# Kernel optimization log

Measured on AMD Instinct MI355X. Metric: run time of the kernel, lower is better.

## Reference

```python
import jax, jax.numpy as jnp
import numpy as np

B, N, D, S, ITERS = 64, 4096, 256, 8, 3
EPS_ATTN = 1e-8
EPS_LN = 1e-5


def layernorm(x, g, b):
    mu = jnp.mean(x, axis=-1, keepdims=True)
    var = jnp.mean(jnp.square(x - mu), axis=-1, keepdims=True)
    return (x - mu) * jax.lax.rsqrt(var + EPS_LN) * g + b


def setup_inputs() -> dict:
    key = jax.random.key(0)
    ks = jax.random.split(key, 12)
    inputs = jax.random.normal(ks[0], (B, N, D), jnp.float32)
    mask = jax.random.randint(ks[1], (B, N), 0, 2) == 1  # bool, True = masked out
    # xavier-normal init for slots parameter [S, D]
    slots_init = jax.random.normal(ks[2], (S, D), jnp.float32) * np.sqrt(2.0 / (S + D))
    w_std = np.sqrt(1.0 / D)
    Wq = jax.random.normal(ks[3], (D, D), jnp.float32) * w_std
    bq = jnp.zeros((D,), jnp.float32)
    Wk = jax.random.normal(ks[4], (D, D), jnp.float32) * w_std
    bk = jnp.zeros((D,), jnp.float32)
    Wv = jax.random.normal(ks[5], (D, D), jnp.float32) * w_std
    bv = jnp.zeros((D,), jnp.float32)
    W1 = jax.random.normal(ks[6], (D, D), jnp.float32) * w_std
    b1 = jnp.zeros((D,), jnp.float32)
    W2 = jax.random.normal(ks[7], (D, D), jnp.float32) * w_std
    b2 = jnp.zeros((D,), jnp.float32)
    g_in, b_in = jnp.ones((D,)), jnp.zeros((D,))
    g_s, b_s = jnp.ones((D,)), jnp.zeros((D,))
    g_m, b_m = jnp.ones((D,)), jnp.zeros((D,))
    g_o, b_o = jnp.ones((D,)), jnp.zeros((D,))
    return {
        "inputs": inputs, "mask": mask, "slots_init": slots_init,
        "g_in": g_in, "b_in": b_in, "g_s": g_s, "b_s": b_s,
        "g_m": g_m, "b_m": b_m, "g_o": g_o, "b_o": b_o,
        "Wq": Wq, "bq": bq, "Wk": Wk, "bk": bk, "Wv": Wv, "bv": bv,
        "W1": W1, "b1": b1, "W2": W2, "b2": b2,
    }


def reference(inputs, mask, slots_init, g_in, b_in, g_s, b_s, g_m, b_m, g_o, b_o,
              Wq, bq, Wk, bk, Wv, bv, W1, b1, W2, b2):
    x = layernorm(inputs, g_in, b_in)            # [B,N,D]
    k = x @ Wk + bk                               # [B,N,D]
    v = x @ Wv + bv                               # [B,N,D]
    slots = jnp.broadcast_to(slots_init, (B, S, D))
    scale = D ** -0.5
    neg_max = -jnp.finfo(inputs.dtype).max
    for _ in range(ITERS):
        slots_prev = slots
        s = layernorm(slots, g_s, b_s)
        q = s @ Wq + bq                           # [B,S,D]
        dots = jnp.einsum('bid,bjd->bij', q, k) * scale   # [B,S,N]
        dots = jnp.where(mask[:, None, :], neg_max, dots)
        attn = jax.nn.softmax(dots, axis=1)       # softmax over slots (unusual axis)
        attn = attn / (jnp.sum(attn, axis=-1, keepdims=True) + EPS_ATTN)
        updates = jnp.einsum('bjd,bij->bid', v, attn)     # [B,S,D]
        slots = slots_prev + updates
        h = layernorm(slots, g_m, b_m)
        h = jax.nn.relu(h @ W1 + b1) @ W2 + b2    # 2-layer MLP
        slots = slots + h
    return layernorm(slots, g_o, b_o)
```

## Files before the change

kernel.cpp:

```cpp
#include <hip/hip_runtime.h>
#include <stdint.h>

#define BB 64
#define NN 4096
#define DD 256
#define SS 8
#define NITER 3
#define NCHUNK 8
#define EPS_LN 1e-5f
#define EPS_ATTN 1e-8f

typedef __attribute__((ext_vector_type(4))) float fvec4;
typedef __attribute__((ext_vector_type(8))) __bf16 bf16x8;
typedef __attribute__((ext_vector_type(8))) unsigned short usvec8;
typedef __attribute__((ext_vector_type(4))) unsigned short usvec4;

__device__ __forceinline__ float bf2f(unsigned short u) {
  return __uint_as_float(((unsigned)u) << 16);
}
__device__ __forceinline__ unsigned short f2bf(float f) {
  unsigned u = __float_as_uint(f);
  u += 0x7FFFu + ((u >> 16) & 1u);
  return (unsigned short)(u >> 16);
}
__device__ __forceinline__ void async_copy16(void* ldsp, const void* gp) {
  __builtin_amdgcn_global_load_lds(
      (const __attribute__((address_space(1))) unsigned int*)gp,
      (__attribute__((address_space(3))) unsigned int*)ldsp, 16, 0, 0);
}

__global__ void k_sinit(const float* __restrict__ slots_init, float* __restrict__ slots) {
  int b = blockIdx.x, t = threadIdx.x;
  const fvec4* src = (const fvec4*)slots_init;
  fvec4* dst = (fvec4*)(slots + (size_t)b * SS * DD);
  for (int j = t; j < SS * DD / 4; j += 256) dst[j] = src[j];
}

__global__ void k_wprepT(const float* __restrict__ Wk, float* __restrict__ WkT) {
  __shared__ float tile[16][17];
  int bx = blockIdx.x, by = blockIdx.y, t = threadIdx.x;
  int r = t >> 4, c = t & 15;
  tile[r][c] = Wk[(size_t)(by * 16 + r) * DD + bx * 16 + c];
  __syncthreads();
  WkT[(size_t)(bx * 16 + r) * DD + by * 16 + c] = tile[c][r];
}

__launch_bounds__(256)
__global__ void k_wcomb(const float* __restrict__ Wq, const float* __restrict__ WkT,
                        const float* __restrict__ bq, const float* __restrict__ bk,
                        float* __restrict__ Wqk, float* __restrict__ bqk,
                        float* __restrict__ wqbk, float* __restrict__ bqbk) {
  __shared__ float wqrow[DD];
  __shared__ float red[4];
  const float sc = 0.0625f;
  int j = blockIdx.x, t = threadIdx.x;
  wqrow[t] = Wq[(size_t)j * DD + t];
  __syncthreads();
  float a = 0.f;
#pragma unroll 4
  for (int dk = 0; dk < DD; dk++) a += wqrow[dk] * WkT[(size_t)dk * DD + t];
  Wqk[(size_t)j * DD + t] = a * sc;
  float c = wqrow[t] * bk[t];
#pragma unroll
  for (int m = 32; m >= 1; m >>= 1) c += __shfl_xor(c, m);
  if ((t & 63) == 0) red[t >> 6] = c;
  __syncthreads();
  if (t == 0) wqbk[j] = sc * (red[0] + red[1] + red[2] + red[3]);
  if (j == 0) {
    float bb = 0.f;
#pragma unroll 4
    for (int dk = 0; dk < DD; dk++) bb += bq[dk] * WkT[(size_t)dk * DD + t];
    bqk[t] = bb * sc;
    __syncthreads();
    float c2 = bq[t] * bk[t];
#pragma unroll
    for (int m = 32; m >= 1; m >>= 1) c2 += __shfl_xor(c2, m);
    if ((t & 63) == 0) red[t >> 6] = c2;
    __syncthreads();
    if (t == 0) bqbk[0] = sc * (red[0] + red[1] + red[2] + red[3]);
  }
}

__launch_bounds__(256)
__global__ void k_lnx(const float* __restrict__ in, const float* __restrict__ g,
                      const float* __restrict__ bt, unsigned short* __restrict__ xbf) {
  int t = threadIdx.x;
  long row = (long)blockIdx.x * 32 + (t >> 3);
  int u = t & 7;
  const float* rp = in + row * DD;
  fvec4 v[8];
  float s = 0.f, s2 = 0.f;
#pragma unroll
  for (int j = 0; j < 8; j++) {
    v[j] = *(const fvec4*)(rp + j * 32 + u * 4);
    s += v[j].x + v[j].y + v[j].z + v[j].w;
    s2 += v[j].x * v[j].x + v[j].y * v[j].y + v[j].z * v[j].z + v[j].w * v[j].w;
  }
  s += __shfl_xor(s, 1); s2 += __shfl_xor(s2, 1);
  s += __shfl_xor(s, 2); s2 += __shfl_xor(s2, 2);
  s += __shfl_xor(s, 4); s2 += __shfl_xor(s2, 4);
  float mu = s / DD;
  float rs = rsqrtf(s2 / DD - mu * mu + EPS_LN);
#pragma unroll
  for (int j = 0; j < 8; j++) {
    fvec4 gg = *(const fvec4*)(g + j * 32 + u * 4);
    fvec4 bb = *(const fvec4*)(bt + j * 32 + u * 4);
    usvec4 o;
    o[0] = f2bf((v[j].x - mu) * rs * gg.x + bb.x);
    o[1] = f2bf((v[j].y - mu) * rs * gg.y + bb.y);
    o[2] = f2bf((v[j].z - mu) * rs * gg.z + bb.z);
    o[3] = f2bf((v[j].w - mu) * rs * gg.w + bb.w);
    *(usvec4*)&xbf[row * DD + j * 32 + u * 4] = o;
  }
}

__launch_bounds__(256, 2)
__global__ void k_slotq2(const float* __restrict__ slots, const float* __restrict__ g_s,
                         const float* __restrict__ b_s, const float* __restrict__ Wqk,
                         const float* __restrict__ bqk, const float* __restrict__ wqbk,
                         const float* __restrict__ bqbk, float* __restrict__ qk,
                         float* __restrict__ qb, float* __restrict__ colsum) {
  __shared__ float sl[SS][DD];
  __shared__ float part[8][SS][32];
  __shared__ float qbp[4][SS];
  int b = blockIdx.x, cg = blockIdx.y, t = threadIdx.x;
  if (cg == 0 && t < SS) colsum[b * SS + t] = 0.f;
  int row = t >> 5, seg = t & 31;
  {
    const float* sp = slots + (size_t)(b * SS + row) * DD + seg * 8;
    float v[8];
    float s = 0.f, s2 = 0.f;
#pragma unroll
    for (int e = 0; e < 8; e++) { v[e] = sp[e]; s += v[e]; s2 += v[e] * v[e]; }
#pragma unroll
    for (int m = 16; m >= 1; m >>= 1) { s += __shfl_xor(s, m); s2 += __shfl_xor(s2, m); }
    float mu = s / DD;
    float rs = rsqrtf(s2 / DD - mu * mu + EPS_LN);
#pragma unroll
    for (int e = 0; e < 8; e++) {
      int d = seg * 8 + e;
      sl[row][d] = (v[e] - mu) * rs * g_s[d] + b_s[d];
    }
  }
  __syncthreads();
  if (cg == 0) {
    float wb = wqbk[t];
    float c8[SS];
#pragma unroll
    for (int i = 0; i < SS; i++) c8[i] = sl[i][t] * wb;
#pragma unroll
    for (int m = 32; m >= 1; m >>= 1)
#pragma unroll
      for (int i = 0; i < SS; i++) c8[i] += __shfl_xor(c8[i], m);
    if ((t & 63) == 0) {
#pragma unroll
      for (int i = 0; i < SS; i++) qbp[t >> 6][i] = c8[i];
    }
  }
  int kq = t >> 5, c = t & 31;
  int colg = cg * 32 + c;
  float a[SS] = {};
#pragma unroll 8
  for (int kk = 0; kk < 32; kk++) {
    int k = kq * 32 + kk;
    float wv = Wqk[(size_t)k * DD + colg];
#pragma unroll
    for (int i = 0; i < SS; i++) a[i] += sl[i][k] * wv;
  }
#pragma unroll
  for (int i = 0; i < SS; i++) part[kq][i][c] = a[i];
  __syncthreads();
  {
    int i = t >> 5, c2 = t & 31;
    float s = 0.f;
#pragma unroll
    for (int kq2 = 0; kq2 < 8; kq2++) s += part[kq2][i][c2];
    int cg2 = cg * 32 + c2;
    qk[(size_t)(b * SS + i) * DD + cg2] = s + bqk[cg2];
  }
  if (cg == 0 && t < SS)
    qb[b * SS + t] = qbp[0][t] + qbp[1][t] + qbp[2][t] + qbp[3][t] + bqbk[0];
}

__launch_bounds__(256, 2)
__global__ void k_attn2(const unsigned short* __restrict__ xbf,
                        const float* __restrict__ qkb, const float* __restrict__ qb,
                        const int* __restrict__ mask,
                        float* __restrict__ colsum, float* __restrict__ upart) {
  __shared__ __attribute__((aligned(16))) unsigned short kt[2][64 * 256];
  __shared__ float aL[2][64 * 9];
  int b = blockIdx.y, chunk = blockIdx.x, t = threadIdx.x;
  int w = t >> 6, lane = t & 63;
  int n_base = chunk * 512;
  int cl15 = lane & 15, hg = lane >> 4;

  bf16x8 qf[8];
  {
    int qrow = cl15 < 8 ? cl15 : 0;
    const float* qp = qkb + (size_t)(b * SS + qrow) * DD;
#pragma unroll
    for (int kst = 0; kst < 8; kst++) {
      int d0 = kst * 32 + hg * 8;
      usvec8 uq;
      if (cl15 < 8) {
        fvec4 q0 = *(const fvec4*)(qp + d0);
        fvec4 q1 = *(const fvec4*)(qp + d0 + 4);
        uq[0] = f2bf(q0.x); uq[1] = f2bf(q0.y); uq[2] = f2bf(q0.z); uq[3] = f2bf(q0.w);
        uq[4] = f2bf(q1.x); uq[5] = f2bf(q1.y); uq[6] = f2bf(q1.z); uq[7] = f2bf(q1.w);
      } else {
        uq = (usvec8)0;
      }
      qf[kst] = __builtin_bit_cast(bf16x8, uq);
    }
  }
  float qadd[4];
#pragma unroll
  for (int e = 0; e < 4; e++) qadd[e] = qb[b * SS + (hg & 1) * 4 + e];

  float acc[SS][8] = {};
  float csum[4] = {};
  int ns = t >> 5;

  auto stage = [&](int c, int bb) {
    int r0 = n_base + c * 64;
#pragma unroll
    for (int j = 0; j < 8; j++) {
      int gidx = w * 512 + j * 64 + lane;
      int row = gidx >> 5, c16 = gidx & 31;
      async_copy16(&kt[bb][gidx * 8],
                   xbf + ((size_t)(b * NN + r0 + row)) * DD + ((c16 ^ (row & 7)) * 8));
    }
  };

  stage(0, 0);
  for (int c = 0; c < 8; c++) {
    int bb = c & 1, pb = c & 1;
    int r0 = n_base + c * 64;
    if (c < 7) {
      stage(c + 1, bb ^ 1);
      asm volatile("s_waitcnt vmcnt(8)" ::: "memory");
    } else {
      asm volatile("s_waitcnt vmcnt(0)" ::: "memory");
    }
    __builtin_amdgcn_sched_barrier(0);
    fvec4 S = {0.f, 0.f, 0.f, 0.f};
    int row_l = w * 16 + cl15;
#pragma unroll
    for (int kst = 0; kst < 8; kst++) {
      int c16 = (kst * 4 + hg) ^ (row_l & 7);
      bf16x8 bfk = *(const bf16x8*)&kt[bb][row_l * 256 + c16 * 8];
      S = __builtin_amdgcn_mfma_f32_16x16x32_bf16(qf[kst], bfk, S, 0, 0, 0);
    }
    S[0] += qadd[0]; S[1] += qadd[1]; S[2] += qadd[2]; S[3] += qadd[3];
    {
      float m4 = fmaxf(fmaxf(S[0], S[1]), fmaxf(S[2], S[3]));
      float mo = __shfl_xor(m4, 16);
      float mx = fmaxf(m4, mo);
      float e0 = __expf(S[0] - mx), e1 = __expf(S[1] - mx);
      float e2 = __expf(S[2] - mx), e3 = __expf(S[3] - mx);
      float s4 = e0 + e1 + e2 + e3;
      float so = __shfl_xor(s4, 16);
      float inv = 1.f / (s4 + so);
      int mk = mask[(size_t)b * NN + r0 + row_l];
      float a0 = mk ? 0.125f : e0 * inv;
      float a1 = mk ? 0.125f : e1 * inv;
      float a2 = mk ? 0.125f : e2 * inv;
      float a3 = mk ? 0.125f : e3 * inv;
      if (lane < 32) {
        csum[0] += a0; csum[1] += a1; csum[2] += a2; csum[3] += a3;
        float* ap = &aL[pb][(w * 16 + cl15) * 9 + hg * 4];
        ap[0] = a0; ap[1] = a1; ap[2] = a2; ap[3] = a3;
      }
    }
    __syncthreads();
#pragma unroll
    for (int s8 = 0; s8 < 8; s8++) {
      int r = s8 * 8 + ns;
      usvec8 vv = *(const usvec8*)&kt[bb][r * 256 + (((t & 31)) ^ (r & 7)) * 8];
      float vf[8];
#pragma unroll
      for (int e = 0; e < 8; e++) vf[e] = bf2f(vv[e]);
#pragma unroll
      for (int i = 0; i < SS; i++) {
        float aw = aL[pb][r * 9 + i];
#pragma unroll
        for (int e = 0; e < 8; e++) acc[i][e] += aw * vf[e];
      }
    }
    __syncthreads();
  }
#pragma unroll
  for (int m = 1; m <= 8; m <<= 1)
#pragma unroll
    for (int e = 0; e < 4; e++) csum[e] += __shfl_xor(csum[e], m);
  if (lane == 0) {
#pragma unroll
    for (int e = 0; e < 4; e++) atomicAdd(&colsum[b * SS + e], csum[e]);
  } else if (lane == 16) {
#pragma unroll
    for (int e = 0; e < 4; e++) atomicAdd(&colsum[b * SS + 4 + e], csum[e]);
  }
#pragma unroll
  for (int i = 0; i < SS; i++)
#pragma unroll
    for (int e = 0; e < 8; e++) acc[i][e] += __shfl_xor(acc[i][e], 32);
  __syncthreads();
  float* red = (float*)&kt[0][0];
  if (lane < 32) {
#pragma unroll
    for (int i = 0; i < SS; i++) {
      fvec4 a0 = {acc[i][0], acc[i][1], acc[i][2], acc[i][3]};
      fvec4 a1 = {acc[i][4], acc[i][5], acc[i][6], acc[i][7]};
      *(fvec4*)&red[(w * SS + i) * DD + lane * 8] = a0;
      *(fvec4*)&red[(w * SS + i) * DD + lane * 8 + 4] = a1;
    }
  }
  __syncthreads();
  int i2 = t >> 5, dsg = (t & 31) * 8;
  float* up = upart + ((size_t)(b * NCHUNK + chunk)) * (SS * DD) + i2 * DD + dsg;
#pragma unroll
  for (int e = 0; e < 8; e++)
    up[e] = red[(0 * SS + i2) * DD + dsg + e] + red[(1 * SS + i2) * DD + dsg + e] +
            red[(2 * SS + i2) * DD + dsg + e] + red[(3 * SS + i2) * DD + dsg + e];
}

__launch_bounds__(256, 2)
__global__ void k_updv(const float* __restrict__ slots, const float* __restrict__ upart,
                       const float* __restrict__ Wv, const float* __restrict__ bv,
                       const float* __restrict__ colsum, float* __restrict__ snbuf) {
  __shared__ float yL[SS][DD];
  __shared__ float part[8][SS][32];
  int b = blockIdx.x, cg = blockIdx.y, t = threadIdx.x;
  {
    int i = t >> 5, seg = t & 31;
    fvec4 sa = {0.f, 0.f, 0.f, 0.f}, sb = {0.f, 0.f, 0.f, 0.f};
#pragma unroll
    for (int c = 0; c < NCHUNK; c++) {
      const float* up = upart + ((size_t)(b * NCHUNK + c)) * (SS * DD) + i * DD + seg * 8;
      fvec4 u0 = *(const fvec4*)up;
      fvec4 u1 = *(const fvec4*)(up + 4);
      sa.x += u0.x; sa.y += u0.y; sa.z += u0.z; sa.w += u0.w;
      sb.x += u1.x; sb.y += u1.y; sb.z += u1.z; sb.w += u1.w;
    }
    *(fvec4*)&yL[i][seg * 8] = sa;
    *(fvec4*)&yL[i][seg * 8 + 4] = sb;
  }
  __syncthreads();
  int kq = t >> 5, c = t & 31;
  int colg = cg * 32 + c;
  float a[SS] = {};
#pragma unroll 8
  for (int kk = 0; kk < 32; kk++) {
    int k = kq * 32 + kk;
    float wv = Wv[(size_t)k * DD + colg];
#pragma unroll
    for (int i = 0; i < SS; i++) a[i] += yL[i][k] * wv;
  }
#pragma unroll
  for (int i = 0; i < SS; i++) part[kq][i][c] = a[i];
  __syncthreads();
  {
    int i = t >> 5, c2 = t & 31;
    float s = 0.f;
#pragma unroll
    for (int kq2 = 0; kq2 < 8; kq2++) s += part[kq2][i][c2];
    int cg2 = cg * 32 + c2;
    float cs = colsum[b * SS + i];
    float csinv = 1.f / (cs + EPS_ATTN);
    size_t idx = (size_t)(b * SS + i) * DD + cg2;
    snbuf[idx] = slots[idx] + (s + bv[cg2] * cs) * csinv;
  }
}

__launch_bounds__(256, 2)
__global__ void k_mlp1(const float* __restrict__ snbuf, const float* __restrict__ g_m,
                       const float* __restrict__ b_m, const float* __restrict__ W1,
                       const float* __restrict__ b1, float* __restrict__ h2g) {
  __shared__ float hL[SS][DD];
  __shared__ float part[8][SS][32];
  int b = blockIdx.x, cg = blockIdx.y, t = threadIdx.x;
  int row = t >> 5, seg = t & 31;
  {
    const float* sp = snbuf + (size_t)(b * SS + row) * DD + seg * 8;
    float v[8], s = 0.f, s2 = 0.f;
#pragma unroll
    for (int e = 0; e < 8; e++) { v[e] = sp[e]; s += v[e]; s2 += v[e] * v[e]; }
#pragma unroll
    for (int m = 16; m >= 1; m >>= 1) { s += __shfl_xor(s, m); s2 += __shfl_xor(s2, m); }
    float mu = s / DD;
    float rs = rsqrtf(s2 / DD - mu * mu + EPS_LN);
#pragma unroll
    for (int e = 0; e < 8; e++) {
      int d = seg * 8 + e;
      hL[row][d] = (v[e] - mu) * rs * g_m[d] + b_m[d];
    }
  }
  __syncthreads();
  int kq = t >> 5, c = t & 31;
  int colg = cg * 32 + c;
  float a[SS] = {};
#pragma unroll 8
  for (int kk = 0; kk < 32; kk++) {
    int k = kq * 32 + kk;
    float wv = W1[(size_t)k * DD + colg];
#pragma unroll
    for (int i = 0; i < SS; i++) a[i] += hL[i][k] * wv;
  }
#pragma unroll
  for (int i = 0; i < SS; i++) part[kq][i][c] = a[i];
  __syncthreads();
  {
    int i = t >> 5, c2 = t & 31;
    float s = 0.f;
#pragma unroll
    for (int kq2 = 0; kq2 < 8; kq2++) s += part[kq2][i][c2];
    int cg2 = cg * 32 + c2;
    h2g[(size_t)(b * SS + i) * DD + cg2] = fmaxf(s + b1[cg2], 0.f);
  }
}

__launch_bounds__(256, 2)
__global__ void k_mlp2(float* __restrict__ slots, const float* __restrict__ snbuf,
                       const float* __restrict__ h2g, const float* __restrict__ W2,
                       const float* __restrict__ b2) {
  __shared__ float h2L[SS][DD];
  __shared__ float part[8][SS][32];
  int b = blockIdx.x, cg = blockIdx.y, t = threadIdx.x;
  {
    const fvec4* src = (const fvec4*)(h2g + (size_t)b * SS * DD);
    fvec4* dst = (fvec4*)h2L;
    for (int j = t; j < SS * DD / 4; j += 256) dst[j] = src[j];
  }
  __syncthreads();
  int kq = t >> 5, c = t & 31;
  int colg = cg * 32 + c;
  float a[SS] = {};
#pragma unroll 8
  for (int kk = 0; kk < 32; kk++) {
    int k = kq * 32 + kk;
    float wv = W2[(size_t)k * DD + colg];
#pragma unroll
    for (int i = 0; i < SS; i++) a[i] += h2L[i][k] * wv;
  }
#pragma unroll
  for (int i = 0; i < SS; i++) part[kq][i][c] = a[i];
  __syncthreads();
  {
    int i = t >> 5, c2 = t & 31;
    float s = 0.f;
#pragma unroll
    for (int kq2 = 0; kq2 < 8; kq2++) s += part[kq2][i][c2];
    int cg2 = cg * 32 + c2;
    size_t idx = (size_t)(b * SS + i) * DD + cg2;
    slots[idx] = snbuf[idx] + s + b2[cg2];
  }
}

__launch_bounds__(256)
__global__ void k_out(const float* __restrict__ slots, const float* __restrict__ g_o,
                      const float* __restrict__ b_o, float* __restrict__ out) {
  int b = blockIdx.x, t = threadIdx.x;
  int row = t >> 5, seg = t & 31;
  const float* sp = slots + (size_t)(b * SS + row) * DD + seg * 8;
  float v[8];
  float s = 0.f, s2 = 0.f;
#pragma unroll
  for (int e = 0; e < 8; e++) { v[e] = sp[e]; s += v[e]; s2 += v[e] * v[e]; }
#pragma unroll
  for (int m = 16; m >= 1; m >>= 1) { s += __shfl_xor(s, m); s2 += __shfl_xor(s2, m); }
  float mu = s / DD;
  float rs = rsqrtf(s2 / DD - mu * mu + EPS_LN);
#pragma unroll
  for (int e = 0; e < 8; e++) {
    int d = seg * 8 + e;
    out[(size_t)(b * SS + row) * DD + d] = (v[e] - mu) * rs * g_o[d] + b_o[d];
  }
}

extern "C" void kernel_launch(void* const* d_in, const int* in_sizes, int n_in,
                              void* d_out, int out_size, void* d_ws, size_t ws_size,
                              hipStream_t stream) {
  (void)in_sizes; (void)n_in; (void)out_size; (void)ws_size;
  const float* inputs = (const float*)d_in[0];
  const int* mask = (const int*)d_in[1];
  const float* slots_init = (const float*)d_in[2];
  const float* g_in = (const float*)d_in[3];
  const float* b_in = (const float*)d_in[4];
  const float* g_s = (const float*)d_in[5];
  const float* b_s = (const float*)d_in[6];
  const float* g_m = (const float*)d_in[7];
  const float* b_m = (const float*)d_in[8];
  const float* g_o = (const float*)d_in[9];
  const float* b_o = (const float*)d_in[10];
  const float* Wq = (const float*)d_in[11];
  const float* bq = (const float*)d_in[12];
  const float* Wk = (const float*)d_in[13];
  const float* bk = (const float*)d_in[14];
  const float* Wv = (const float*)d_in[15];
  const float* bv = (const float*)d_in[16];
  const float* W1 = (const float*)d_in[17];
  const float* b1 = (const float*)d_in[18];
  const float* W2 = (const float*)d_in[19];
  const float* b2 = (const float*)d_in[20];
  float* out = (float*)d_out;

  char* ws = (char*)d_ws;
  size_t off = 0;
  auto alloc = [&](size_t bytes) -> void* {
    void* p = ws + off;
    off += (bytes + 255) & ~(size_t)255;
    return p;
  };
  unsigned short* xbf = (unsigned short*)alloc((size_t)BB * NN * DD * 2);
  float* WkT = (float*)alloc((size_t)DD * DD * 4);
  float* Wqk = (float*)alloc((size_t)DD * DD * 4);
  float* bqk = (float*)alloc((size_t)DD * 4);
  float* wqbk = (float*)alloc((size_t)DD * 4);
  float* bqbk = (float*)alloc(4);
  float* qk = (float*)alloc((size_t)BB * SS * DD * 4);
  float* qb = (float*)alloc((size_t)BB * SS * 4);
  float* slots = (float*)alloc((size_t)BB * SS * DD * 4);
  float* snbuf = (float*)alloc((size_t)BB * SS * DD * 4);
  float* h2g = (float*)alloc((size_t)BB * SS * DD * 4);
  float* upart = (float*)alloc((size_t)BB * NCHUNK * SS * DD * 4);
  float* colsum = (float*)alloc((size_t)BB * SS * 4);

  k_sinit<<<dim3(BB), dim3(256), 0, stream>>>(slots_init, slots);
  k_wprepT<<<dim3(16, 16), dim3(256), 0, stream>>>(Wk, WkT);
  k_wcomb<<<dim3(DD), dim3(256), 0, stream>>>(Wq, WkT, bq, bk, Wqk, bqk, wqbk, bqbk);
  k_lnx<<<dim3(BB * NN / 32), dim3(256), 0, stream>>>(inputs, g_in, b_in, xbf);

  for (int it = 0; it < NITER; ++it) {
    k_slotq2<<<dim3(BB, 8), dim3(256), 0, stream>>>(slots, g_s, b_s, Wqk, bqk, wqbk, bqbk,
                                                    qk, qb, colsum);
    k_attn2<<<dim3(NCHUNK, BB), dim3(256), 0, stream>>>(xbf, qk, qb, mask, colsum, upart);
    k_updv<<<dim3(BB, 8), dim3(256), 0, stream>>>(slots, upart, Wv, bv, colsum, snbuf);
    k_mlp1<<<dim3(BB, 8), dim3(256), 0, stream>>>(snbuf, g_m, b_m, W1, b1, h2g);
    k_mlp2<<<dim3(BB, 8), dim3(256), 0, stream>>>(slots, snbuf, h2g, W2, b2);
  }
  k_out<<<dim3(BB), dim3(256), 0, stream>>>(slots, g_o, b_o, out);
}
```

Before: 392.0 us.

## Fuse slot-attention iterations into one cooperative persistent kernel with per-batch flags

Replaces the per-iteration chain of attention, value-update, MLP and query kernels with a single cooperative kernel of 256 blocks (4 chunks per batch). The last-arriving block per batch runs the slot-side update (Wv projection, layernorm, MLP, next query) while the other blocks spin on a ready flag. Slots and column sums are double-buffered. This removes many kernel launches and global round-trips, but cuts attention parallelism per batch from 8 chunks to 4 and serialises the slot-side work onto one block per batch.

```diff
diff --git a/kernel.cpp b/kernel.cpp
--- a/kernel.cpp
+++ b/kernel.cpp
@@ -6,6 +6,7 @@
 #define DD 256
 #define SS 8
 #define NITER 3
+#define NCH 4
 #define NCHUNK 8
 #define EPS_LN 1e-5f
 #define EPS_ATTN 1e-8f
@@ -29,11 +30,16 @@
       (__attribute__((address_space(3))) unsigned int*)ldsp, 16, 0, 0);
 }
 
-__global__ void k_sinit(const float* __restrict__ slots_init, float* __restrict__ slots) {
+__global__ void k_sinit(const float* __restrict__ slots_init, float* __restrict__ slots,
+                        int* __restrict__ sync) {
   int b = blockIdx.x, t = threadIdx.x;
   const fvec4* src = (const fvec4*)slots_init;
   fvec4* dst = (fvec4*)(slots + (size_t)b * SS * DD);
   for (int j = t; j < SS * DD / 4; j += 256) dst[j] = src[j];
+  if (t < NITER) {
+    sync[t * BB + b] = 0;
+    sync[NITER * BB + t * BB + b] = 0;
+  }
 }
 
 __global__ void k_wprepT(const float* __restrict__ Wk, float* __restrict__ WkT) {
@@ -180,6 +186,370 @@
   }
   if (cg == 0 && t < SS)
     qb[b * SS + t] = qbp[0][t] + qbp[1][t] + qbp[2][t] + qbp[3][t] + bqbk[0];
+}
+
+static __device__ __forceinline__ void attn_chunk_body(
+    int ab, int ck, const unsigned short* __restrict__ xbf,
+    const float* __restrict__ qk, const float* __restrict__ qb,
+    const int* __restrict__ mask, float* __restrict__ colsum,
+    float* __restrict__ upart, unsigned short* kt0, unsigned short* kt1,
+    float* aL0, float* aL1) {
+  int t = threadIdx.x;
+  int w = t >> 6, lane = t & 63;
+  int cl15 = lane & 15, hg = lane >> 4;
+  int ns = t >> 5;
+  int n_base = ck * 1024;
+
+  bf16x8 qf[8];
+  {
+    int qrow = cl15 < 8 ? cl15 : 0;
+    const float* qp = qk + (size_t)(ab * SS + qrow) * DD;
+#pragma unroll
+    for (int kst = 0; kst < 8; kst++) {
+      int d0 = kst * 32 + hg * 8;
+      usvec8 uq;
+      if (cl15 < 8) {
+        fvec4 q0 = *(const fvec4*)(qp + d0);
+        fvec4 q1 = *(const fvec4*)(qp + d0 + 4);
+        uq[0] = f2bf(q0.x); uq[1] = f2bf(q0.y); uq[2] = f2bf(q0.z); uq[3] = f2bf(q0.w);
+        uq[4] = f2bf(q1.x); uq[5] = f2bf(q1.y); uq[6] = f2bf(q1.z); uq[7] = f2bf(q1.w);
+      } else {
+        uq = (usvec8)0;
+      }
+      qf[kst] = __builtin_bit_cast(bf16x8, uq);
+    }
+  }
+  float qadd[4];
+#pragma unroll
+  for (int e = 0; e < 4; e++) qadd[e] = qb[ab * SS + (hg & 1) * 4 + e];
+
+  float acc[SS][8] = {};
+  float csum[4] = {};
+
+  auto stage = [&](int c, int bbuf) {
+    unsigned short* ktb = bbuf ? kt1 : kt0;
+    int r0 = n_base + c * 64;
+#pragma unroll
+    for (int j = 0; j < 8; j++) {
+      int gidx = w * 512 + j * 64 + lane;
+      int row = gidx >> 5, c16 = gidx & 31;
+      async_copy16(&ktb[gidx * 8],
+                   xbf + ((size_t)(ab * NN + r0 + row)) * DD + ((c16 ^ (row & 7)) * 8));
+    }
+  };
+
+  stage(0, 0);
+  for (int c = 0; c < 16; c++) {
+    int bbuf = c & 1;
+    unsigned short* ktb = bbuf ? kt1 : kt0;
+    float* aLb = bbuf ? aL1 : aL0;
+    int r0 = n_base + c * 64;
+    if (c < 15) {
+      stage(c + 1, bbuf ^ 1);
+      asm volatile("s_waitcnt vmcnt(8)" ::: "memory");
+    } else {
+      asm volatile("s_waitcnt vmcnt(0)" ::: "memory");
+    }
+    __builtin_amdgcn_sched_barrier(0);
+    fvec4 S = {0.f, 0.f, 0.f, 0.f};
+    int row_l = w * 16 + cl15;
+#pragma unroll
+    for (int kst = 0; kst < 8; kst++) {
+      int c16 = (kst * 4 + hg) ^ (row_l & 7);
+      bf16x8 bfk = *(const bf16x8*)&ktb[row_l * 256 + c16 * 8];
+      S = __builtin_amdgcn_mfma_f32_16x16x32_bf16(qf[kst], bfk, S, 0, 0, 0);
+    }
+    S[0] += qadd[0]; S[1] += qadd[1]; S[2] += qadd[2]; S[3] += qadd[3];
+    {
+      float m4 = fmaxf(fmaxf(S[0], S[1]), fmaxf(S[2], S[3]));
+      float mo = __shfl_xor(m4, 16);
+      float mx = fmaxf(m4, mo);
+      float e0 = __expf(S[0] - mx), e1 = __expf(S[1] - mx);
+      float e2 = __expf(S[2] - mx), e3 = __expf(S[3] - mx);
+      float s4 = e0 + e1 + e2 + e3;
+      float so = __shfl_xor(s4, 16);
+      float inv = 1.f / (s4 + so);
+      int mk = mask[(size_t)ab * NN + r0 + row_l];
+      float a0 = mk ? 0.125f : e0 * inv;
+      float a1 = mk ? 0.125f : e1 * inv;
+      float a2 = mk ? 0.125f : e2 * inv;
+      float a3 = mk ? 0.125f : e3 * inv;
+      if (lane < 32) {
+        csum[0] += a0; csum[1] += a1; csum[2] += a2; csum[3] += a3;
+        float* ap = &aLb[(w * 16 + cl15) * 9 + hg * 4];
+        ap[0] = a0; ap[1] = a1; ap[2] = a2; ap[3] = a3;
+      }
+    }
+    __syncthreads();
+#pragma unroll
+    for (int s8 = 0; s8 < 8; s8++) {
+      int r = s8 * 8 + ns;
+      usvec8 vv = *(const usvec8*)&ktb[r * 256 + (((t & 31)) ^ (r & 7)) * 8];
+      float vf[8];
+#pragma unroll
+      for (int e = 0; e < 8; e++) vf[e] = bf2f(vv[e]);
+#pragma unroll
+      for (int i = 0; i < SS; i++) {
+        float aw = aLb[r * 9 + i];
+#pragma unroll
+        for (int e = 0; e < 8; e++) acc[i][e] += aw * vf[e];
+      }
+    }
+    __syncthreads();
+  }
+#pragma unroll
+  for (int m = 1; m <= 8; m <<= 1)
+#pragma unroll
+    for (int e = 0; e < 4; e++) csum[e] += __shfl_xor(csum[e], m);
+  if (lane == 0) {
+#pragma unroll
+    for (int e = 0; e < 4; e++) atomicAdd(&colsum[ab * SS + e], csum[e]);
+  } else if (lane == 16) {
+#pragma unroll
+    for (int e = 0; e < 4; e++) atomicAdd(&colsum[ab * SS + 4 + e], csum[e]);
+  }
+#pragma unroll
+  for (int i = 0; i < SS; i++)
+#pragma unroll
+    for (int e = 0; e < 8; e++) acc[i][e] += __shfl_xor(acc[i][e], 32);
+  __syncthreads();
+  float* red = (float*)kt0;
+  if (lane < 32) {
+#pragma unroll
+    for (int i = 0; i < SS; i++) {
+      fvec4 a0 = {acc[i][0], acc[i][1], acc[i][2], acc[i][3]};
+      fvec4 a1 = {acc[i][4], acc[i][5], acc[i][6], acc[i][7]};
+      *(fvec4*)&red[(w * SS + i) * DD + lane * 8] = a0;
+      *(fvec4*)&red[(w * SS + i) * DD + lane * 8 + 4] = a1;
+    }
+  }
+  __syncthreads();
+  int i2 = t >> 5, dsg = (t & 31) * 8;
+  float* up = upart + ((size_t)(ab * NCH + ck)) * (SS * DD) + i2 * DD + dsg;
+#pragma unroll
+  for (int e = 0; e < 8; e++)
+    up[e] = red[(0 * SS + i2) * DD + dsg + e] + red[(1 * SS + i2) * DD + dsg + e] +
+            red[(2 * SS + i2) * DD + dsg + e] + red[(3 * SS + i2) * DD + dsg + e];
+}
+
+static __device__ __forceinline__ void slotside_body(
+    int b, const float* __restrict__ sl_rd, float* __restrict__ sl_wr,
+    const float* __restrict__ upart, const float* __restrict__ Wv,
+    const float* __restrict__ bv, const float* __restrict__ cs_rd,
+    float* __restrict__ cs_wr, const float* __restrict__ g_m,
+    const float* __restrict__ b_m, const float* __restrict__ W1,
+    const float* __restrict__ b1, const float* __restrict__ W2,
+    const float* __restrict__ b2, const float* __restrict__ g_s,
+    const float* __restrict__ b_s, const float* __restrict__ Wqk,
+    const float* __restrict__ bqk, const float* __restrict__ wqbk,
+    const float* __restrict__ bqbk, float* __restrict__ qk,
+    float* __restrict__ qb, int do_q,
+    float* yL, float* snL, float* hL, float* h2L, float* qbp) {
+  int t = threadIdx.x;
+  int w = t >> 6, lane = t & 63;
+  float cs[SS], csinv[SS];
+#pragma unroll
+  for (int i = 0; i < SS; i++) {
+    cs[i] = cs_rd[b * SS + i];
+    csinv[i] = 1.f / (cs[i] + EPS_ATTN);
+  }
+#pragma unroll
+  for (int i = 0; i < SS; i++) {
+    float s = 0.f;
+#pragma unroll
+    for (int c = 0; c < NCH; c++)
+      s += upart[((size_t)(b * NCH + c)) * (SS * DD) + i * DD + t];
+    yL[i * DD + t] = s;
+  }
+  __syncthreads();
+  {
+    float a[SS] = {};
+#pragma unroll 8
+    for (int k = 0; k < DD; k += 4) {
+      float w0 = Wv[(size_t)(k + 0) * DD + t];
+      float w1 = Wv[(size_t)(k + 1) * DD + t];
+      float w2 = Wv[(size_t)(k + 2) * DD + t];
+      float w3 = Wv[(size_t)(k + 3) * DD + t];
+#pragma unroll
+      for (int i = 0; i < SS; i++)
+        a[i] += yL[i * DD + k] * w0 + yL[i * DD + k + 1] * w1 +
+                yL[i * DD + k + 2] * w2 + yL[i * DD + k + 3] * w3;
+    }
+    float bvt = bv[t];
+#pragma unroll
+    for (int i = 0; i < SS; i++)
+      snL[i * DD + t] = sl_rd[(size_t)b * SS * DD + i * DD + t] + (a[i] + bvt * cs[i]) * csinv[i];
+  }
+  __syncthreads();
+  {
+    int row = t >> 5, seg = t & 31;
+    float v[8], s = 0.f, s2 = 0.f;
+#pragma unroll
+    for (int e = 0; e < 8; e++) { v[e] = snL[row * DD + seg * 8 + e]; s += v[e]; s2 += v[e] * v[e]; }
+#pragma unroll
+    for (int m = 16; m >= 1; m >>= 1) { s += __shfl_xor(s, m); s2 += __shfl_xor(s2, m); }
+    float mu = s / DD, rs = rsqrtf(s2 / DD - mu * mu + EPS_LN);
+#pragma unroll
+    for (int e = 0; e < 8; e++) {
+      int d = seg * 8 + e;
+      hL[row * DD + d] = (v[e] - mu) * rs * g_m[d] + b_m[d];
+    }
+  }
+  __syncthreads();
+  {
+    float a[SS] = {};
+#pragma unroll 8
+    for (int k = 0; k < DD; k += 4) {
+      float w0 = W1[(size_t)(k + 0) * DD + t];
+      float w1 = W1[(size_t)(k + 1) * DD + t];
+      float w2 = W1[(size_t)(k + 2) * DD + t];
+      float w3 = W1[(size_t)(k + 3) * DD + t];
+#pragma unroll
+      for (int i = 0; i < SS; i++)
+        a[i] += hL[i * DD + k] * w0 + hL[i * DD + k + 1] * w1 +
+                hL[i * DD + k + 2] * w2 + hL[i * DD + k + 3] * w3;
+    }
+    float b1t = b1[t];
+#pragma unroll
+    for (int i = 0; i < SS; i++) h2L[i * DD + t] = fmaxf(a[i] + b1t, 0.f);
+  }
+  __syncthreads();
+  {
+    float a[SS] = {};
+#pragma unroll 8
+    for (int k = 0; k < DD; k += 4) {
+      float w0 = W2[(size_t)(k + 0) * DD + t];
+      float w1 = W2[(size_t)(k + 1) * DD + t];
+      float w2 = W2[(size_t)(k + 2) * DD + t];
+      float w3 = W2[(size_t)(k + 3) * DD + t];
+#pragma unroll
+      for (int i = 0; i < SS; i++)
+        a[i] += h2L[i * DD + k] * w0 + h2L[i * DD + k + 1] * w1 +
+                h2L[i * DD + k + 2] * w2 + h2L[i * DD + k + 3] * w3;
+    }
+    float b2t = b2[t];
+#pragma unroll
+    for (int i = 0; i < SS; i++) {
+      float v = snL[i * DD + t] + a[i] + b2t;
+      yL[i * DD + t] = v;
+      sl_wr[(size_t)b * SS * DD + i * DD + t] = v;
+    }
+  }
+  if (t < SS) cs_wr[b * SS + t] = 0.f;
+  if (!do_q) return;
+  __syncthreads();
+  {
+    int row = t >> 5, seg = t & 31;
+    float v[8], s = 0.f, s2 = 0.f;
+#pragma unroll
+    for (int e = 0; e < 8; e++) { v[e] = yL[row * DD + seg * 8 + e]; s += v[e]; s2 += v[e] * v[e]; }
+#pragma unroll
+    for (int m = 16; m >= 1; m >>= 1) { s += __shfl_xor(s, m); s2 += __shfl_xor(s2, m); }
+    float mu = s / DD, rs = rsqrtf(s2 / DD - mu * mu + EPS_LN);
+#pragma unroll
+    for (int e = 0; e < 8; e++) {
+      int d = seg * 8 + e;
+      snL[row * DD + d] = (v[e] - mu) * rs * g_s[d] + b_s[d];
+    }
+  }
+  __syncthreads();
+  {
+    float wb = wqbk[t];
+    float c8[SS];
+#pragma unroll
+    for (int i = 0; i < SS; i++) c8[i] = snL[i * DD + t] * wb;
+#pragma unroll
+    for (int m = 32; m >= 1; m >>= 1)
+#pragma unroll
+      for (int i = 0; i < SS; i++) c8[i] += __shfl_xor(c8[i], m);
+    if (lane == 0) {
+#pragma unroll
+      for (int i = 0; i < SS; i++) qbp[w * SS + i] = c8[i];
+    }
+  }
+  {
+    float a[SS] = {};
+#pragma unroll 8
+    for (int k = 0; k < DD; k += 4) {
+      float w0 = Wqk[(size_t)(k + 0) * DD + t];
+      float w1 = Wqk[(size_t)(k + 1) * DD + t];
+      float w2 = Wqk[(size_t)(k + 2) * DD + t];
+      float w3 = Wqk[(size_t)(k + 3) * DD + t];
+#pragma unroll
+      for (int i = 0; i < SS; i++)
+        a[i] += snL[i * DD + k] * w0 + snL[i * DD + k + 1] * w1 +
+                snL[i * DD + k + 2] * w2 + snL[i * DD + k + 3] * w3;
+    }
+    float bqkt = bqk[t];
+#pragma unroll
+    for (int i = 0; i < SS; i++) qk[(size_t)(b * SS + i) * DD + t] = a[i] + bqkt;
+  }
+  __syncthreads();
+  if (t < SS) qb[b * SS + t] = qbp[0 * SS + t] + qbp[1 * SS + t] + qbp[2 * SS + t] + qbp[3 * SS + t] + bqbk[0];
+}
+
+__launch_bounds__(256, 2)
+__global__ void k_iter2(const unsigned short* __restrict__ xbf, const int* __restrict__ mask,
+                        float* __restrict__ qk, float* __restrict__ qb,
+                        float* __restrict__ slots, float* __restrict__ colsum,
+                        float* __restrict__ upart,
+                        const float* __restrict__ Wv, const float* __restrict__ bv,
+                        const float* __restrict__ g_m, const float* __restrict__ b_m,
+                        const float* __restrict__ W1, const float* __restrict__ b1,
+                        const float* __restrict__ W2, const float* __restrict__ b2,
+                        const float* __restrict__ g_s, const float* __restrict__ b_s,
+                        const float* __restrict__ Wqk, const float* __restrict__ bqk,
+                        const float* __restrict__ wqbk, const float* __restrict__ bqbk,
+                        int* __restrict__ sync) {
+  __shared__ __attribute__((aligned(16))) unsigned short kt0[64 * 256];
+  __shared__ __attribute__((aligned(16))) unsigned short kt1[64 * 256];
+  __shared__ float aL0[64 * 9], aL1[64 * 9];
+  __shared__ float qbp[4 * SS];
+  __shared__ int sh_elect;
+  const size_t SLOT_SZ = (size_t)BB * SS * DD;
+  const size_t CS_SZ = (size_t)BB * SS;
+  int* arrive = sync;
+  int* ready = sync + NITER * BB;
+  int bid = blockIdx.x, t = threadIdx.x;
+  int ab = bid >> 2, ck = bid & 3;
+
+  for (int it = 0; it < NITER; ++it) {
+    float* cs_rd = colsum + (size_t)(it & 1) * CS_SZ;
+    float* cs_wr = colsum + (size_t)((it + 1) & 1) * CS_SZ;
+    const float* sl_rd = slots + (size_t)(it & 1) * SLOT_SZ;
+    float* sl_wr = slots + (size_t)((it + 1) & 1) * SLOT_SZ;
+    int do_q = (it < NITER - 1);
+
+    attn_chunk_body(ab, ck, xbf, qk, qb, mask, cs_rd, upart, kt0, kt1, aL0, aL1);
+
+    __threadfence();
+    __syncthreads();
+    if (t == 0) {
+      int old = atomicAdd(&arrive[it * BB + ab], 1);
+      sh_elect = (old == NCH - 1) ? 1 : 0;
+    }
+    __syncthreads();
+    if (sh_elect) {
+      __threadfence();
+      slotside_body(ab, sl_rd, sl_wr, upart, Wv, bv, cs_rd, cs_wr, g_m, b_m, W1, b1,
+                    W2, b2, g_s, b_s, Wqk, bqk, wqbk, bqbk, qk, qb, do_q,
+                    (float*)kt0, (float*)kt0 + SS * DD, (float*)kt1,
+                    (float*)kt1 + SS * DD, qbp);
+      __threadfence();
+      __syncthreads();
+      if (t == 0)
+        __hip_atomic_store(&ready[it * BB + ab], 1, __ATOMIC_RELEASE, __HIP_MEMORY_SCOPE_AGENT);
+    }
+    if (it < NITER - 1) {
+      if (t == 0) {
+        while (__hip_atomic_load(&ready[it * BB + ab], __ATOMIC_ACQUIRE,
+                                 __HIP_MEMORY_SCOPE_AGENT) == 0)
+          __builtin_amdgcn_s_sleep(8);
+      }
+      __syncthreads();
+      __threadfence();
+    }
+  }
 }
 
 __launch_bounds__(256, 2)
@@ -519,24 +889,42 @@
   float* bqbk = (float*)alloc(4);
   float* qk = (float*)alloc((size_t)BB * SS * DD * 4);
   float* qb = (float*)alloc((size_t)BB * SS * 4);
-  float* slots = (float*)alloc((size_t)BB * SS * DD * 4);
+  float* slots = (float*)alloc((size_t)2 * BB * SS * DD * 4);
   float* snbuf = (float*)alloc((size_t)BB * SS * DD * 4);
   float* h2g = (float*)alloc((size_t)BB * SS * DD * 4);
   float* upart = (float*)alloc((size_t)BB * NCHUNK * SS * DD * 4);
-  float* colsum = (float*)alloc((size_t)BB * SS * 4);
-
-  k_sinit<<<dim3(BB), dim3(256), 0, stream>>>(slots_init, slots);
+  float* colsum = (float*)alloc((size_t)2 * BB * SS * 4);
+  int* sync = (int*)alloc((size_t)2 * NITER * BB * 4);
+
+  const size_t SLOT_SZ = (size_t)BB * SS * DD;
+
+  k_sinit<<<dim3(BB), dim3(256), 0, stream>>>(slots_init, slots, sync);
   k_wprepT<<<dim3(16, 16), dim3(256), 0, stream>>>(Wk, WkT);
   k_wcomb<<<dim3(DD), dim3(256), 0, stream>>>(Wq, WkT, bq, bk, Wqk, bqk, wqbk, bqbk);
   k_lnx<<<dim3(BB * NN / 32), dim3(256), 0, stream>>>(inputs, g_in, b_in, xbf);
-
-  for (int it = 0; it < NITER; ++it) {
-    k_slotq2<<<dim3(BB, 8), dim3(256), 0, stream>>>(slots, g_s, b_s, Wqk, bqk, wqbk, bqbk,
-                                                    qk, qb, colsum);
-    k_attn2<<<dim3(NCHUNK, BB), dim3(256), 0, stream>>>(xbf, qk, qb, mask, colsum, upart);
-    k_updv<<<dim3(BB, 8), dim3(256), 0, stream>>>(slots, upart, Wv, bv, colsum, snbuf);
-    k_mlp1<<<dim3(BB, 8), dim3(256), 0, stream>>>(snbuf, g_m, b_m, W1, b1, h2g);
-    k_mlp2<<<dim3(BB, 8), dim3(256), 0, stream>>>(slots, snbuf, h2g, W2, b2);
-  }
-  k_out<<<dim3(BB), dim3(256), 0, stream>>>(slots, g_o, b_o, out);
-}
+  k_slotq2<<<dim3(BB, 8), dim3(256), 0, stream>>>(slots, g_s, b_s, Wqk, bqk, wqbk, bqbk,
+                                                  qk, qb, colsum);
+
+  void* args[] = {(void*)&xbf, (void*)&mask, (void*)&qk, (void*)&qb, (void*)&slots,
+                  (void*)&colsum, (void*)&upart, (void*)&Wv, (void*)&bv, (void*)&g_m,
+                  (void*)&b_m, (void*)&W1, (void*)&b1, (void*)&W2, (void*)&b2,
+                  (void*)&g_s, (void*)&b_s, (void*)&Wqk, (void*)&bqk, (void*)&wqbk,
+                  (void*)&bqbk, (void*)&sync};
+  hipError_t cerr = hipLaunchCooperativeKernel((const void*)k_iter2, dim3(BB * NCH),
+                                               dim3(256), args, 0, stream);
+  if (cerr == hipSuccess) {
+    k_out<<<dim3(BB), dim3(256), 0, stream>>>(slots + (NITER & 1) * SLOT_SZ, g_o, b_o, out);
+  } else {
+    (void)hipGetLastError();
+    for (int it = 0; it < NITER; ++it) {
+      if (it > 0)
+        k_slotq2<<<dim3(BB, 8), dim3(256), 0, stream>>>(slots, g_s, b_s, Wqk, bqk, wqbk,
+                                                        bqbk, qk, qb, colsum);
+      k_attn2<<<dim3(NCHUNK, BB), dim3(256), 0, stream>>>(xbf, qk, qb, mask, colsum, upart);
+      k_updv<<<dim3(BB, 8), dim3(256), 0, stream>>>(slots, upart, Wv, bv, colsum, snbuf);
+      k_mlp1<<<dim3(BB, 8), dim3(256), 0, stream>>>(snbuf, g_m, b_m, W1, b1, h2g);
+      k_mlp2<<<dim3(BB, 8), dim3(256), 0, stream>>>(slots, snbuf, h2g, W2, b2);
+    }
+    k_out<<<dim3(BB), dim3(256), 0, stream>>>(slots, g_o, b_o, out);
+  }
+}
```

Measured after the change: 1.489 ms. 3.8x slower.
